# Kernel optimization log

Hardware: AMD Instinct MI355X
Metric: run time of the kernel (lower is better)

## Reference

```python
import jax, jax.numpy as jnp
import numpy as np

H8, W8 = 64, 64
H4, W4 = 128, 128
C_LAT, C_HI = 256, 128
N_Q = 1024
ORIG_H, ORIG_W = 512, 512
NUM_ITERS = 4
TEMP = 20.0
DIM = 4 + C_HI + C_LAT        # 388 mixer output dim
IN_DIM = DIM + 3 * 49         # 535 mixer input dim
HID = 512


def _unit(v):
    return v / jnp.sqrt(jnp.maximum(jnp.sum(v * v, axis=-1, keepdims=True), 1e-12))


def setup_inputs() -> dict:
    key = jax.random.key(0)
    ks = jax.random.split(key, 20)
    fg = _unit(jax.random.normal(ks[0], (1, H8, W8, C_LAT), jnp.float32))
    hg = _unit(jax.random.normal(ks[1], (1, H4, W4, C_HI), jnp.float32))
    qf = _unit(jax.random.normal(ks[2], (1, N_Q, C_LAT), jnp.float32))
    hq = _unit(jax.random.normal(ks[3], (1, N_Q, C_HI), jnp.float32))
    p = lambda k, s, sc=0.05: sc * jax.random.normal(k, s, jnp.float32)
    return dict(
        feature_grid=fg, hires_feats_grid=hg, query_feats=qf, hires_query_feats=hq,
        hid1_w=p(ks[4], (16, 1, 3, 3)), hid1_b=jnp.zeros((16,), jnp.float32),
        hid2_w=p(ks[5], (1, 16, 3, 3)), hid2_b=jnp.zeros((1,), jnp.float32),
        hid3_w=p(ks[6], (32, 16, 3, 3)), hid3_b=jnp.zeros((32,), jnp.float32),
        hid4_w=p(ks[7], (32, 16)), hid4_b=jnp.zeros((16,), jnp.float32),
        occ_w=p(ks[8], (16, 2)), occ_b=jnp.zeros((2,), jnp.float32),
        mix_in_w=p(ks[9], (IN_DIM, HID), 0.02), mix_in_b=jnp.zeros((HID,), jnp.float32),
        mix_out_w=p(ks[10], (HID, DIM), 0.02), mix_out_b=jnp.zeros((DIM,), jnp.float32),
    )


def _conv2d(x, w, b, stride, pad):
    y = jax.lax.conv_general_dilated(x, w, (stride, stride), pad,
                                     dimension_numbers=('NCHW', 'OIHW', 'NCHW'))
    return y + b[None, :, None, None]


def _bilinear_sample(grid, coords):
    # grid [H,W,C]; coords [..., 2] as (y, x); edge-clamped bilinear gather.
    H, W = grid.shape[0], grid.shape[1]
    y, x = coords[..., 0], coords[..., 1]
    y0f, x0f = jnp.floor(y), jnp.floor(x)
    wy, wx = (y - y0f)[..., None], (x - x0f)[..., None]
    y0 = jnp.clip(y0f.astype(jnp.int32), 0, H - 1)
    y1 = jnp.clip(y0f.astype(jnp.int32) + 1, 0, H - 1)
    x0 = jnp.clip(x0f.astype(jnp.int32), 0, W - 1)
    x1 = jnp.clip(x0f.astype(jnp.int32) + 1, 0, W - 1)
    g00, g01 = grid[y0, x0], grid[y0, x1]
    g10, g11 = grid[y1, x0], grid[y1, x1]
    return (g00 * (1 - wy) * (1 - wx) + g01 * (1 - wy) * wx
            + g10 * wy * (1 - wx) + g11 * wy * wx)


def _forward(fg, hg, qf, hq, hid1_w, hid1_b, hid2_w, hid2_b, hid3_w, hid3_b,
             hid4_w, hid4_b, occ_w, occ_b, mix_in_w, mix_in_b, mix_out_w, mix_out_b):
    # --- tracks_from_cost_volume ---
    cv = jnp.einsum('bnc,bhwc->bnhw', qf, fg)                 # [1,N,64,64]
    b, n, h, w = cv.shape
    x = cv.reshape(b * n, 1, h, w)
    occ_map = jax.nn.relu(_conv2d(x, hid1_w, hid1_b, 1, 'SAME'))   # [bn,16,h,w]
    pmap = _conv2d(occ_map, hid2_w, hid2_b, 1, 'SAME').reshape(b * n, h * w)
    heat = jax.nn.softmax(pmap * TEMP, axis=-1).reshape(b * n, h, w)
    ey = jnp.einsum('bhw,h->b', heat, jnp.arange(h, dtype=jnp.float32))
    ex = jnp.einsum('bhw,w->b', heat, jnp.arange(w, dtype=jnp.float32))
    points = jnp.stack([ex * (ORIG_W / w), ey * (ORIG_H / h)], -1).reshape(b, n, 2)
    op = jnp.pad(occ_map, ((0, 0), (0, 0), (0, 2), (0, 2)))
    o3 = jax.nn.relu(_conv2d(op, hid3_w, hid3_b, 2, 'VALID'))
    o3 = o3.mean((-1, -2))                                     # [bn,32]
    o3 = jax.nn.relu(o3 @ hid4_w + hid4_b)
    o3 = (o3 @ occ_w + occ_b).reshape(b, n, 2)
    occ, expd = o3[..., 0], o3[..., 1]

    # --- iterative pips refinement ---
    cy, cx = jnp.meshgrid(jnp.arange(-3, 4), jnp.arange(-3, 4), indexing='ij')
    ctx = jnp.stack([cy, cx], -1).reshape(-1, 2).astype(jnp.float32)   # [49,2] (dy,dx)
    fg_avg = fg.reshape(1, H8 // 2, 2, W8 // 2, 2, C_LAT).mean((2, 4))
    pyramid = [hg, fg, fg_avg]
    feats = jnp.concatenate([hq, qf], -1)                      # [1,N,384]
    pos = points
    for it in range(NUM_ITERS):
        if it == 0:
            queries = [hq[0], qf[0], qf[0]]
        else:
            queries = [feats[0, :, :C_HI], feats[0, :, C_HI:], feats[0, :, C_HI:]]
        corrs = []
        for grid, q in zip(pyramid, queries):
            gh, gw = grid.shape[1], grid.shape[2]
            scale = jnp.array([gw / ORIG_W, gh / ORIG_H], jnp.float32)
            c = (pos[0] * scale)[:, ::-1]                      # (x,y)->(y,x), [N,2]
            coords2 = c[:, None, :] + ctx[None]                # [N,49,2]
            nb = _bilinear_sample(grid[0], coords2)            # [N,49,C]
            corrs.append(jnp.einsum('nsc,nc->ns', nb, q))
        corrs = jnp.concatenate(corrs, -1)[None]               # [1,N,147]
        mlp_in = jnp.concatenate([jnp.zeros_like(pos), occ[..., None],
                                  expd[..., None], feats, corrs], -1)
        res = jax.nn.gelu(mlp_in @ mix_in_w + mix_in_b) @ mix_out_w + mix_out_b
        pos = pos + res[..., :2]
        occ = occ + res[..., 2]
        expd = expd + res[..., 3]
        feats = feats + res[..., 4:]
    return jnp.concatenate([pos, occ[..., None], expd[..., None]], -1)  # [1,N,4]


def reference(feature_grid, hires_feats_grid, query_feats, hires_query_feats,
              hid1_w, hid1_b, hid2_w, hid2_b, hid3_w, hid3_b, hid4_w, hid4_b,
              occ_w, occ_b, mix_in_w, mix_in_b, mix_out_w, mix_out_b):
    return _forward(feature_grid, hires_feats_grid, query_feats, hires_query_feats,
                    hid1_w, hid1_b, hid2_w, hid2_b, hid3_w, hid3_b, hid4_w, hid4_b,
                    occ_w, occ_b, mix_in_w, mix_in_b, mix_out_w, mix_out_b)
```

## Files before the change

### kernel.cpp

```cpp
#include <hip/hip_runtime.h>
#include <hip/hip_bf16.h>
#include <math.h>


#define NQ 1024
#define TEMPF 20.0f
#define DIMV 388
#define INDIM 535
#define KPAD 544
#define HID 512

#define WS_CVB     0
#define WS_WIT     2097152
#define WS_WOT     2236416
#define WS_FG16    2351104
#define WS_HG16    2875392
#define WS_AV16    3923968
#define WS_FGAVG   4194304
#define WS_POS     (WS_FGAVG + 262144)
#define WS_OCC     (WS_POS + NQ*2)
#define WS_EXPD    (WS_OCC + NQ)
#define WS_FEATS   (WS_EXPD + NQ)
#define WS_MLPIN   (WS_FEATS + NQ*384)
#define WS_HIDDEN  (WS_MLPIN + NQ*KPAD)
#define WS_W3B     (WS_HIDDEN + NQ*HID)
#define WS_W2B     (WS_W3B + 2560)
#define WS_PART    (WS_MLPIN + 278528)
#define WS_SUM3    WS_HIDDEN

#define CVP 68
#define ROWP 2368

typedef __attribute__((ext_vector_type(8))) short bf16x8;
typedef __attribute__((ext_vector_type(4))) float f32x4;

union BU8 { uint4 u; __hip_bfloat16 h[8]; };

__device__ __forceinline__ int occ_off(int r, int idx, int c) {
  int o = idx * 32 + c * 2;
  o ^= ((idx >> 2) & 3) << 4;
  return r * ROWP + o;
}

__global__ __launch_bounds__(256) void k_prep_cv(
    const float* __restrict__ fg, const float* __restrict__ hg,
    const float* __restrict__ qf, const float* __restrict__ hq,
    const float* __restrict__ w3, const float* __restrict__ w2,
    const float* __restrict__ wi, const float* __restrict__ wo,
    float* __restrict__ ws) {
  __shared__ __hip_bfloat16 A_s[32 * 32];
  __shared__ __hip_bfloat16 B_s[64 * 32];
  const int bx = blockIdx.x;
  const int t = threadIdx.x;

  if (bx >= 2048) {
    int i = (bx - 2048) * 256 + t;
    if (i < 262144) {
      int c = i & 255, ox = (i >> 8) & 31, oy = i >> 13;
      const float* b = fg + (((oy * 2) * 64 + ox * 2) << 8) + c;
      float av = 0.25f * (b[0] + b[256] + b[16384] + b[16384 + 256]);
      ((__hip_bfloat16*)(ws + WS_AV16))[i] = __float2bfloat16(av);
    } else if (i < 655360) {
      int j = i - 262144;
      int n = j / 384, c = j - n * 384;
      float v = (c < 128) ? hq[n * 128 + c] : qf[n * 256 + c - 128];
      ws[WS_FEATS + j] = v;
      __hip_bfloat16* mi = (__hip_bfloat16*)(ws + WS_MLPIN);
      mi[n * KPAD + 4 + c] = __float2bfloat16(v);
      if (c == 0) {
        mi[n * KPAD + 0] = __float2bfloat16(0.f);
        mi[n * KPAD + 1] = __float2bfloat16(0.f);
      }
    } else if (i < 660480) {
      int j = i - 655360;
      int e = j & 7, qd = (j >> 3) & 3, nl = (j >> 5) & 15;
      int nt = (j >> 9) & 1, kt = j >> 10;
      int k = kt * 32 + qd * 8 + e;
      int ic = k & 15, tap = k >> 4;
      int oc = nt * 16 + nl;
      float v = (tap < 9) ? w3[(oc * 16 + ic) * 9 + tap] : 0.f;
      ((__hip_bfloat16*)(ws + WS_W3B))[j] = __float2bfloat16(v);
    } else if (i < 663040) {
      int j = i - 660480;
      int e = j & 7, qd = (j >> 3) & 3, kt = j >> 9;
      int k = kt * 32 + qd * 8 + e;
      int ch = k & 15, tap = k >> 4;
      float v = (tap < 9) ? w2[ch * 9 + tap] : 0.f;
      ((__hip_bfloat16*)(ws + WS_W2B))[j] = __float2bfloat16(v);
    } else if (i < 1187328) {
      ws[WS_SUM3 + (i - 663040)] = 0.f;
    } else if (i < 1465856) {
      int j = i - 1187328;
      int n = j / KPAD, k = j - n * KPAD;
      float v = (k < INDIM) ? wi[k * HID + n] : 0.f;
      ((__hip_bfloat16*)(ws + WS_WIT))[j] = __float2bfloat16(v);
    } else if (i < 1695232) {
      int j = i - 1465856;
      int n = j >> 9, k = j & 511;
      float v = (n < DIMV) ? wo[k * DIMV + n] : 0.f;
      ((__hip_bfloat16*)(ws + WS_WOT))[j] = __float2bfloat16(v);
    } else if (i < 1957376) {
      int j = (i - 1695232) * 4;
      float4 v = *(const float4*)&fg[j];
      union { __hip_bfloat16 h[4]; uint2 u; } pk;
      pk.h[0] = __float2bfloat16(v.x); pk.h[1] = __float2bfloat16(v.y);
      pk.h[2] = __float2bfloat16(v.z); pk.h[3] = __float2bfloat16(v.w);
      *(uint2*)(((__hip_bfloat16*)(ws + WS_FG16)) + j) = pk.u;
    } else {
      int j = (i - 1957376) * 4;
      float4 v = *(const float4*)&hg[j];
      union { __hip_bfloat16 h[4]; uint2 u; } pk;
      pk.h[0] = __float2bfloat16(v.x); pk.h[1] = __float2bfloat16(v.y);
      pk.h[2] = __float2bfloat16(v.z); pk.h[3] = __float2bfloat16(v.w);
      *(uint2*)(((__hip_bfloat16*)(ws + WS_HG16)) + j) = pk.u;
    }
    return;
  }

  const int wv = t >> 6, lane = t & 63;
  const int wm = wv & 1, wn = wv >> 1;
  const int quad = lane >> 4, nl = lane & 15;
  const int p0 = (bx & 63) * 64, m0 = (bx >> 6) * 32;
  f32x4 acc0 = {0.f, 0.f, 0.f, 0.f};
  f32x4 acc1 = {0.f, 0.f, 0.f, 0.f};

  for (int k0 = 0; k0 < 256; k0 += 32) {
    {
      int r = t >> 3, c = t & 7;
      float4 v = *(const float4*)&qf[(m0 + r) * 256 + k0 + c * 4];
      union { __hip_bfloat16 h[4]; uint2 u; } pk;
      pk.h[0] = __float2bfloat16(v.x); pk.h[1] = __float2bfloat16(v.y);
      pk.h[2] = __float2bfloat16(v.z); pk.h[3] = __float2bfloat16(v.w);
      *(uint2*)&A_s[r * 32 + c * 4] = pk.u;
    }
    {
      int r = t >> 2, c = t & 3;
      const float* src = &fg[(p0 + r) * 256 + k0 + c * 8];
      float4 v0 = *(const float4*)src;
      float4 v1 = *(const float4*)(src + 4);
      union { __hip_bfloat16 h[8]; uint4 u; } pk;
      pk.h[0] = __float2bfloat16(v0.x); pk.h[1] = __float2bfloat16(v0.y);
      pk.h[2] = __float2bfloat16(v0.z); pk.h[3] = __float2bfloat16(v0.w);
      pk.h[4] = __float2bfloat16(v1.x); pk.h[5] = __float2bfloat16(v1.y);
      pk.h[6] = __float2bfloat16(v1.z); pk.h[7] = __float2bfloat16(v1.w);
      *(uint4*)&B_s[r * 32 + c * 8] = pk.u;
    }
    __syncthreads();
    bf16x8 a = *(const bf16x8*)&A_s[(16 * wm + nl) * 32 + quad * 8];
    bf16x8 b0 = *(const bf16x8*)&B_s[(32 * wn + nl) * 32 + quad * 8];
    bf16x8 b1 = *(const bf16x8*)&B_s[(32 * wn + 16 + nl) * 32 + quad * 8];
    acc0 = __builtin_amdgcn_mfma_f32_16x16x32_bf16(a, b0, acc0, 0, 0, 0);
    acc1 = __builtin_amdgcn_mfma_f32_16x16x32_bf16(a, b1, acc1, 0, 0, 0);
    __syncthreads();
  }
  __hip_bfloat16* cvb = (__hip_bfloat16*)ws;
#pragma unroll
  for (int nt = 0; nt < 2; nt++) {
    int n = p0 + 32 * wn + nt * 16 + nl;
#pragma unroll
    for (int r = 0; r < 4; r++) {
      int m = m0 + 16 * wm + quad * 4 + r;
      cvb[m * 4096 + n] = __float2bfloat16(nt ? acc1[r] : acc0[r]);
    }
  }
}

__global__ __launch_bounds__(256, 5) void k_head_stripe(
    const float* __restrict__ h1w, const float* __restrict__ h1b,
    const float* __restrict__ h2b, const float* __restrict__ h3b,
    float* __restrict__ ws) {
  __shared__ float cvs[8 * CVP];
  __shared__ float4 occ_t4[6 * ROWP / 16];
  char* occ_t = (char*)occ_t4;

  const int bx = blockIdx.x;
  const int q = bx >> 4, st = bx & 15;
  const int y0 = st * 4;
  const int t = threadIdx.x;
  const int wv = t >> 6, lane = t & 63;
  const int role = (wv + bx) & 3;
  const __hip_bfloat16* cvb = (const __hip_bfloat16*)ws + q * 4096;

  if (t < 192) {
    int r = t >> 5, j = t & 31;
    int off = r * ROWP + ((j < 16) ? j * 8 : 2176 + (j - 16) * 8);
    *(uint2*)(occ_t + off) = make_uint2(0u, 0u);
  }
  if (st == 0 || st == 15) {
    int r = (st == 0) ? 0 : 5;
    for (int i = t; i < 288; i += 256)
      *(uint2*)(occ_t + r * ROWP + i * 8) = make_uint2(0u, 0u);
  }
#pragma unroll
  for (int j = 0; j < 2; j++) {
    int i = t + 256 * j;
    int lr = i >> 6, x = i & 63;
    int g = y0 - 2 + lr;
    cvs[lr * CVP + x + 1] =
        (g >= 0 && g < 64) ? __bfloat162float(cvb[g * 64 + x]) : 0.f;
  }
  if (t < 32) {
    int rr = t >> 2, c = t & 3;
    cvs[rr * CVP + ((c == 0) ? 0 : (64 + c))] = 0.f;
  }
  __syncthreads();

  {
    const int x = lane;
    const int chg = wv * 4;
    float w1r[4][9], b1r[4];
#pragma unroll
    for (int k = 0; k < 4; k++) {
      b1r[k] = h1b[chg + k];
#pragma unroll
      for (int j = 0; j < 9; j++) w1r[k][j] = h1w[(chg + k) * 9 + j];
    }
    float win[3][3];
#pragma unroll
    for (int j = 0; j < 3; j++) {
      const float* cp = &cvs[j * CVP + x];
      win[j][0] = cp[0]; win[j][1] = cp[1]; win[j][2] = cp[2];
    }
    for (int r = 0; r < 6; r++) {
      if (r > 0) {
#pragma unroll
        for (int c = 0; c < 3; c++) { win[0][c] = win[1][c]; win[1][c] = win[2][c]; }
        const float* cp = &cvs[(r + 2) * CVP + x];
        win[2][0] = cp[0]; win[2][1] = cp[1]; win[2][2] = cp[2];
      }
      int yo = y0 - 1 + r;
      if (yo >= 0 && yo <= 63) {
        union { __hip_bfloat16 h[4]; uint2 u; } pk;
#pragma unroll
        for (int k = 0; k < 4; k++) {
          float a = b1r[k];
#pragma unroll
          for (int ky = 0; ky < 3; ky++)
            a += w1r[k][3 * ky] * win[ky][0] + w1r[k][3 * ky + 1] * win[ky][1] +
                 w1r[k][3 * ky + 2] * win[ky][2];
          pk.h[k] = __float2bfloat16(fmaxf(a, 0.f));
        }
        *(uint2*)(occ_t + occ_off(r, x + 4, chg)) = pk.u;
      }
    }
  }
  __syncthreads();

  const int nl = lane & 15;
  const int qd = lane >> 4, qh = qd >> 1, ql = qd & 1;

  if (role == 1 || role == 2) {
    const __hip_bfloat16* W3B = (const __hip_bfloat16*)(ws + WS_W3B);
    const int oyl = role - 1;
    f32x4 acc00 = {0.f,0.f,0.f,0.f}, acc01 = {0.f,0.f,0.f,0.f};
    f32x4 acc10 = {0.f,0.f,0.f,0.f}, acc11 = {0.f,0.f,0.f,0.f};
#pragma unroll
    for (int kt = 0; kt < 5; kt++) {
      int tap = kt * 2 + qh;
      bf16x8 a0, a1;
      if (tap < 9) {
        int ky = (tap >= 6) ? 2 : ((tap >= 3) ? 1 : 0);
        int kx = tap - 3 * ky;
        int R = 2 * oyl + 1 + ky;
        int idx0 = 4 + kx + 2 * nl;
        a0 = *(const bf16x8*)(occ_t + occ_off(R, idx0, ql * 8));
        a1 = *(const bf16x8*)(occ_t + occ_off(R, idx0 + 32, ql * 8));
      } else {
        a0 = (bf16x8){0, 0, 0, 0, 0, 0, 0, 0};
        a1 = a0;
      }
      bf16x8 b0 = *(const bf16x8*)&W3B[((kt * 2 + 0) * 16 + nl) * 32 + qd * 8];
      bf16x8 b1 = *(const bf16x8*)&W3B[((kt * 2 + 1) * 16 + nl) * 32 + qd * 8];
      acc00 = __builtin_amdgcn_mfma_f32_16x16x32_bf16(a0, b0, acc00, 0, 0, 0);
      acc01 = __builtin_amdgcn_mfma_f32_16x16x32_bf16(a0, b1, acc01, 0, 0, 0);
      acc10 = __builtin_amdgcn_mfma_f32_16x16x32_bf16(a1, b0, acc10, 0, 0, 0);
      acc11 = __builtin_amdgcn_mfma_f32_16x16x32_bf16(a1, b1, acc11, 0, 0, 0);
    }
    float bb0 = h3b[nl], bb1 = h3b[16 + nl];
    float s0 = 0.f, s1 = 0.f;
#pragma unroll
    for (int r = 0; r < 4; r++) {
      s0 += fmaxf(acc00[r] + bb0, 0.f) + fmaxf(acc10[r] + bb0, 0.f);
      s1 += fmaxf(acc01[r] + bb1, 0.f) + fmaxf(acc11[r] + bb1, 0.f);
    }
    s0 += __shfl_xor(s0, 16); s0 += __shfl_xor(s0, 32);
    s1 += __shfl_xor(s1, 16); s1 += __shfl_xor(s1, 32);
    if (lane < 16) {
      atomicAdd(&ws[WS_SUM3 + (q * 16 + st) * 32 + nl], s0);
      atomicAdd(&ws[WS_SUM3 + (q * 16 + st) * 32 + 16 + nl], s1);
    }
  } else {
    const int rl0 = (role == 3) ? 2 : 0;
    const __hip_bfloat16* W2B = (const __hip_bfloat16*)(ws + WS_W2B);
    bf16x8 wb0 = *(const bf16x8*)&W2B[(0 * 16 + nl) * 32 + qd * 8];
    bf16x8 wb1 = *(const bf16x8*)&W2B[(1 * 16 + nl) * 32 + qd * 8];
    bf16x8 wb2 = *(const bf16x8*)&W2B[(2 * 16 + nl) * 32 + qd * 8];
    bf16x8 wb3 = *(const bf16x8*)&W2B[(3 * 16 + nl) * 32 + qd * 8];
    bf16x8 wb4 = *(const bf16x8*)&W2B[(4 * 16 + nl) * 32 + qd * 8];
    f32x4 pa0 = {0.f,0.f,0.f,0.f}, pa1 = {0.f,0.f,0.f,0.f};
    f32x4 pa2 = {0.f,0.f,0.f,0.f}, pa3 = {0.f,0.f,0.f,0.f};
    f32x4 pa4 = {0.f,0.f,0.f,0.f}, pa5 = {0.f,0.f,0.f,0.f};
    f32x4 pa6 = {0.f,0.f,0.f,0.f}, pa7 = {0.f,0.f,0.f,0.f};

#define H2STEP(ACC, ROW, XT, KT, WB)                                         \
    {                                                                        \
      int tap = (KT) * 2 + qh;                                               \
      bf16x8 a;                                                              \
      if (tap < 9) {                                                         \
        int ky = (tap >= 6) ? 2 : ((tap >= 3) ? 1 : 0);                      \
        int kx = tap - 3 * ky;                                               \
        a = *(const bf16x8*)(occ_t +                                         \
            occ_off((ROW) + ky, (XT) + nl + 3 + kx, ql * 8));                \
      } else { a = (bf16x8){0, 0, 0, 0, 0, 0, 0, 0}; }                       \
      ACC = __builtin_amdgcn_mfma_f32_16x16x32_bf16(a, WB, ACC, 0, 0, 0);    \
    }
#define H2TILE(ACC, ROW, XT)                                                 \
    H2STEP(ACC, ROW, XT, 0, wb0) H2STEP(ACC, ROW, XT, 1, wb1)                \
    H2STEP(ACC, ROW, XT, 2, wb2) H2STEP(ACC, ROW, XT, 3, wb3)                \
    H2STEP(ACC, ROW, XT, 4, wb4)

    H2TILE(pa0, rl0, 0)      H2TILE(pa1, rl0, 16)
    H2TILE(pa2, rl0, 32)     H2TILE(pa3, rl0, 48)
    H2TILE(pa4, rl0 + 1, 0)  H2TILE(pa5, rl0 + 1, 16)
    H2TILE(pa6, rl0 + 1, 32) H2TILE(pa7, rl0 + 1, 48)
#undef H2TILE
#undef H2STEP

    const float bb = h2b[0];
    float mg = -1e30f;
#pragma unroll
    for (int r = 0; r < 4; r++) {
      mg = fmaxf(mg, fmaxf(fmaxf(pa0[r], pa1[r]), fmaxf(pa2[r], pa3[r])));
      mg = fmaxf(mg, fmaxf(fmaxf(pa4[r], pa5[r]), fmaxf(pa6[r], pa7[r])));
    }
    mg = (mg + bb) * TEMPF;
    mg = fmaxf(mg, __shfl_xor(mg, 16));
    mg = fmaxf(mg, __shfl_xor(mg, 32));
    float sa = 0.f, sb = 0.f, sx = 0.f;
    const float fq = (float)(qd * 4);
#pragma unroll
    for (int r = 0; r < 4; r++) {
      float xr = fq + (float)r;
      float e;
      e = __expf((pa0[r] + bb) * TEMPF - mg); sa += e; sx += e * (xr + 0.f);
      e = __expf((pa1[r] + bb) * TEMPF - mg); sa += e; sx += e * (xr + 16.f);
      e = __expf((pa2[r] + bb) * TEMPF - mg); sa += e; sx += e * (xr + 32.f);
      e = __expf((pa3[r] + bb) * TEMPF - mg); sa += e; sx += e * (xr + 48.f);
      e = __expf((pa4[r] + bb) * TEMPF - mg); sb += e; sx += e * (xr + 0.f);
      e = __expf((pa5[r] + bb) * TEMPF - mg); sb += e; sx += e * (xr + 16.f);
      e = __expf((pa6[r] + bb) * TEMPF - mg); sb += e; sx += e * (xr + 32.f);
      e = __expf((pa7[r] + bb) * TEMPF - mg); sb += e; sx += e * (xr + 48.f);
    }
    float ya = (float)(y0 + rl0);
    float s = sa + sb;
    float sy = ya * sa + (ya + 1.f) * sb;
    s += __shfl_xor(s, 16); sx += __shfl_xor(sx, 16); sy += __shfl_xor(sy, 16);
    s += __shfl_xor(s, 32); sx += __shfl_xor(sx, 32); sy += __shfl_xor(sy, 32);
    if (lane == 0) {
      int slot = q * 32 + st * 2 + ((role == 3) ? 1 : 0);
      *(float4*)&ws[WS_PART + slot * 4] = make_float4(mg, s, sx, sy);
    }
  }
}

__global__ __launch_bounds__(256) void k_merge(
    const float* __restrict__ w4, const float* __restrict__ b4,
    const float* __restrict__ w5, const float* __restrict__ b5,
    float* __restrict__ ws) {
  __shared__ float sums_s[4][32];
  __shared__ float o4s[4][16];
  int t = threadIdx.x, wv = t >> 6, lane = t & 63;
  int q = blockIdx.x * 4 + wv;

  float M = -1e30f, S = 0.f, SX = 0.f, SY = 0.f;
  if (lane < 32) {
    float4 pv = *(const float4*)&ws[WS_PART + (q * 32 + lane) * 4];
    M = pv.x; S = pv.y; SX = pv.z; SY = pv.w;
  }
#pragma unroll
  for (int off = 1; off < 64; off <<= 1) {
    float Mo = __shfl_xor(M, off), So = __shfl_xor(S, off);
    float SXo = __shfl_xor(SX, off), SYo = __shfl_xor(SY, off);
    float Mn = fmaxf(M, Mo);
    float c1 = __expf(M - Mn), c2 = __expf(Mo - Mn);
    S = S * c1 + So * c2; SX = SX * c1 + SXo * c2; SY = SY * c1 + SYo * c2;
    M = Mn;
  }
  if (lane == 0) {
    ws[WS_POS + q * 2 + 0] = (SX / S) * 8.0f;
    ws[WS_POS + q * 2 + 1] = (SY / S) * 8.0f;
  }

  int ch = lane & 31, half = lane >> 5;
  float sm = 0.f;
#pragma unroll
  for (int s8 = 0; s8 < 8; s8++)
    sm += ws[WS_SUM3 + (q * 16 + half * 8 + s8) * 32 + ch];
  sm += __shfl_xor(sm, 32);
  if (lane < 32) sums_s[wv][lane] = sm * (1.f / 1024.f);
  __syncthreads();
  if (lane < 16) {
    float a = b4[lane];
#pragma unroll
    for (int i = 0; i < 32; i++) a += sums_s[wv][i] * w4[i * 16 + lane];
    o4s[wv][lane] = fmaxf(a, 0.f);
  }
  __syncthreads();
  if (lane < 2) {
    float r = b5[lane];
#pragma unroll
    for (int j = 0; j < 16; j++) r += o4s[wv][j] * w5[j * 2 + lane];
    __hip_bfloat16* mi = (__hip_bfloat16*)(ws + WS_MLPIN);
    if (lane == 0) { ws[WS_OCC + q] = r;  mi[q * KPAD + 2] = __float2bfloat16(r); }
    else           { ws[WS_EXPD + q] = r; mi[q * KPAD + 3] = __float2bfloat16(r); }
  }
}

__global__ __launch_bounds__(256) void k_corr(float* __restrict__ ws) {
  __shared__ float qs[384];
  __shared__ float dbuf[3][64];
  int t = threadIdx.x;
  int wv = t >> 6, lane = t & 63;
  int cl = lane & 15, sub = lane >> 4;
  int n = blockIdx.x;
  const float* feats = ws + WS_FEATS + n * 384;
  float posx = ws[WS_POS + n * 2 + 0];
  float posy = ws[WS_POS + n * 2 + 1];
  __hip_bfloat16* mi = (__hip_bfloat16*)(ws + WS_MLPIN) + n * KPAD;

  for (int col = t; col < 384; col += 256) qs[col] = feats[col];
  __syncthreads();

  float qh[8], qq[16];
#pragma unroll
  for (int j = 0; j < 8; j++) qh[j] = qs[cl * 8 + j];
#pragma unroll
  for (int j = 0; j < 16; j++) qq[j] = qs[128 + cl * 16 + j];

  const __hip_bfloat16* G0 = (const __hip_bfloat16*)(ws + WS_HG16);
  const __hip_bfloat16* G1 = (const __hip_bfloat16*)(ws + WS_FG16);
  const __hip_bfloat16* G2 = (const __hip_bfloat16*)(ws + WS_AV16);

#pragma unroll
  for (int L = 0; L < 3; L++) {
    const __hip_bfloat16* grid;
    int Hg, Wg;
    float scl;
    if (L == 0)      { grid = G0; Hg = 128; Wg = 128; scl = 0.25f; }
    else if (L == 1) { grid = G1; Hg = 64;  Wg = 64;  scl = 0.125f; }
    else             { grid = G2; Hg = 32;  Wg = 32;  scl = 0.0625f; }
    float cy = posy * scl, cx = posx * scl;
    int iy = (int)floorf(cy), ix = (int)floorf(cx);
#pragma unroll
    for (int g = 0; g < 4; g++) {
      int p = wv * 16 + g * 4 + sub;
      int a = p >> 3, b = p & 7;
      int row = iy + a - 3; row = row < 0 ? 0 : (row > Hg - 1 ? Hg - 1 : row);
      int col = ix + b - 3; col = col < 0 ? 0 : (col > Wg - 1 ? Wg - 1 : col);
      float acc = 0.f;
      if (L == 0) {
        BU8 g0; g0.u = *(const uint4*)(grid + (row * Wg + col) * 128 + cl * 8);
#pragma unroll
        for (int j = 0; j < 8; j++) acc += __bfloat162float(g0.h[j]) * qh[j];
      } else {
        const __hip_bfloat16* gp = grid + (row * Wg + col) * 256 + cl * 16;
        BU8 g0, g1;
        g0.u = *(const uint4*)gp;
        g1.u = *(const uint4*)(gp + 8);
#pragma unroll
        for (int j = 0; j < 8; j++) {
          acc += __bfloat162float(g0.h[j]) * qq[j];
          acc += __bfloat162float(g1.h[j]) * qq[8 + j];
        }
      }
      acc += __shfl_xor(acc, 1);
      acc += __shfl_xor(acc, 2);
      acc += __shfl_xor(acc, 4);
      acc += __shfl_xor(acc, 8);
      if (cl == 0) dbuf[L][p] = acc;
    }
  }
  __syncthreads();

  if (t < 147) {
    int L = t / 49, s = t - L * 49;
    int sa = s / 7, sb = s - sa * 7;
    float scl = (L == 0) ? 0.25f : ((L == 1) ? 0.125f : 0.0625f);
    float cy = posy * scl, cx = posx * scl;
    float wy = cy - floorf(cy), wx = cx - floorf(cx);
    int i00 = sa * 8 + sb;
    float d00 = dbuf[L][i00], d01 = dbuf[L][i00 + 1];
    float d10 = dbuf[L][i00 + 8], d11 = dbuf[L][i00 + 9];
    float corr = (1.f - wy) * (1.f - wx) * d00 + (1.f - wy) * wx * d01 +
                 wy * (1.f - wx) * d10 + wy * wx * d11;
    mi[388 + t] = __float2bfloat16(corr);
  }
}

__device__ __forceinline__ float gelu_tanh(float x) {
  float z = 0.7978845608028654f * (x + 0.044715f * x * x * x);
  z = fminf(fmaxf(z, -15.f), 15.f);
  float e = __expf(2.f * z);
  float th = (e - 1.f) / (e + 1.f);
  return 0.5f * x * (1.f + th);
}

__global__ __launch_bounds__(256) void k_mix1(
    const float* __restrict__ bias, float* __restrict__ ws) {
  const int t = threadIdx.x;
  const int wv = t >> 6, lane = t & 63;
  const int nt = blockIdx.x * 4 + wv;
  const int mt = blockIdx.y;
  const int m0 = mt * 16, n0 = nt * 16;
  const int nl = lane & 15, quad = lane >> 4;
  const unsigned short* Abf = (const unsigned short*)(ws + WS_MLPIN);
  const unsigned short* WIT = (const unsigned short*)(ws + WS_WIT);
  const unsigned short* ap = &Abf[(m0 + nl) * KPAD + quad * 8];
  const unsigned short* bp = &WIT[(n0 + nl) * KPAD + quad * 8];
  f32x4 acc = {0.f, 0.f, 0.f, 0.f};
#pragma unroll
  for (int ks = 0; ks < 17; ks++) {
    bf16x8 a = *(const bf16x8*)(ap + ks * 32);
    bf16x8 b = *(const bf16x8*)(bp + ks * 32);
    acc = __builtin_amdgcn_mfma_f32_16x16x32_bf16(a, b, acc, 0, 0, 0);
  }
  __hip_bfloat16* Hd = (__hip_bfloat16*)(ws + WS_HIDDEN);
  int nn = n0 + nl;
  float bv = bias[nn];
#pragma unroll
  for (int r = 0; r < 4; r++) {
    int m = m0 + quad * 4 + r;
    Hd[m * HID + nn] = __float2bfloat16(gelu_tanh(acc[r] + bv));
  }
}

__global__ __launch_bounds__(256) void k_mix2(
    const float* __restrict__ bias, float* __restrict__ ws,
    float* __restrict__ out) {
  const int t = threadIdx.x;
  const int wv = t >> 6, lane = t & 63;
  const int nt = blockIdx.x * 4 + wv;
  const int mt = blockIdx.y;
  const int m0 = mt * 16, n0 = nt * 16;
  const int nl = lane & 15, quad = lane >> 4;
  const unsigned short* Abf = (const unsigned short*)(ws + WS_HIDDEN);
  const unsigned short* WOT = (const unsigned short*)(ws + WS_WOT);
  const unsigned short* ap = &Abf[(m0 + nl) * HID + quad * 8];
  const unsigned short* bp = &WOT[(n0 + nl) * HID + quad * 8];
  f32x4 acc = {0.f, 0.f, 0.f, 0.f};
#pragma unroll
  for (int ks = 0; ks < 16; ks++) {
    bf16x8 a = *(const bf16x8*)(ap + ks * 32);
    bf16x8 b = *(const bf16x8*)(bp + ks * 32);
    acc = __builtin_amdgcn_mfma_f32_16x16x32_bf16(a, b, acc, 0, 0, 0);
  }

  int col = n0 + nl;
  if (col < DIMV) {
    float bv = bias[col];
    __hip_bfloat16* mib = (__hip_bfloat16*)(ws + WS_MLPIN);
#pragma unroll
    for (int r = 0; r < 4; r++) {
      int m = m0 + quad * 4 + r;
      float rr = acc[r] + bv;
      if (col < 2) {
        float v = ws[WS_POS + m * 2 + col] + rr;
        ws[WS_POS + m * 2 + col] = v;
        out[m * 4 + col] = v;
      } else if (col == 2) {
        float v = ws[WS_OCC + m] + rr;
        ws[WS_OCC + m] = v;
        out[m * 4 + 2] = v;
        mib[m * KPAD + 2] = __float2bfloat16(v);
      } else if (col == 3) {
        float v = ws[WS_EXPD + m] + rr;
        ws[WS_EXPD + m] = v;
        out[m * 4 + 3] = v;
        mib[m * KPAD + 3] = __float2bfloat16(v);
      } else {
        float v = ws[WS_FEATS + m * 384 + (col - 4)] + rr;
        ws[WS_FEATS + m * 384 + (col - 4)] = v;
        mib[m * KPAD + col] = __float2bfloat16(v);
      }
    }
  }
}

extern "C" void kernel_launch(void* const* d_in, const int* in_sizes, int n_in,
                              void* d_out, int out_size, void* d_ws, size_t ws_size,
                              hipStream_t stream) {
  const float* fg = (const float*)d_in[0];
  const float* hg = (const float*)d_in[1];
  const float* qf = (const float*)d_in[2];
  const float* hq = (const float*)d_in[3];
  const float* w1 = (const float*)d_in[4];
  const float* b1 = (const float*)d_in[5];
  const float* w2 = (const float*)d_in[6];
  const float* b2 = (const float*)d_in[7];
  const float* w3 = (const float*)d_in[8];
  const float* b3 = (const float*)d_in[9];
  const float* w4 = (const float*)d_in[10];
  const float* b4 = (const float*)d_in[11];
  const float* w5 = (const float*)d_in[12];
  const float* b5 = (const float*)d_in[13];
  const float* wi = (const float*)d_in[14];
  const float* bi = (const float*)d_in[15];
  const float* wo = (const float*)d_in[16];
  const float* bo = (const float*)d_in[17];
  float* ws = (float*)d_ws;
  float* out = (float*)d_out;

  k_prep_cv<<<11742, 256, 0, stream>>>(fg, hg, qf, hq, w3, w2, wi, wo, ws);
  k_head_stripe<<<16384, 256, 0, stream>>>(w1, b1, b2, b3, ws);
  k_merge<<<256, 256, 0, stream>>>(w4, b4, w5, b5, ws);
  for (int it = 0; it < 4; it++) {
    k_corr<<<1024, 256, 0, stream>>>(ws);
    k_mix1<<<dim3(8, 64), 256, 0, stream>>>(bi, ws);
    k_mix2<<<dim3(7, 64), 256, 0, stream>>>(bo, ws, out);
  }
}
```

Measured before the change: 298.2 us.

## Fuse merge, correlation and mixer MLP iterations into one persistent kernel

Replaces the merge kernel and the four-iteration loop of correlation, mixer-in and mixer-out launches with a single kernel where each block owns 8 queries and keeps their state, MLP inputs and hidden activations in LDS. This removes many kernel launches and the global round trips for intermediate buffers between stages. In exchange only 128 blocks run, half of each 16-row MFMA tile is padding, and every block re-streams the full mixer weight matrices from L2 each iteration.

```diff
diff --git a/kernel.cpp b/kernel.cpp
--- a/kernel.cpp
+++ b/kernel.cpp
@@ -30,6 +30,8 @@
 
 #define CVP 68
 #define ROWP 2368
+#define MIP 552
+#define HP  520
 
 typedef __attribute__((ext_vector_type(8))) short bf16x8;
 typedef __attribute__((ext_vector_type(4))) float f32x4;
@@ -363,140 +365,6 @@
   }
 }
 
-__global__ __launch_bounds__(256) void k_merge(
-    const float* __restrict__ w4, const float* __restrict__ b4,
-    const float* __restrict__ w5, const float* __restrict__ b5,
-    float* __restrict__ ws) {
-  __shared__ float sums_s[4][32];
-  __shared__ float o4s[4][16];
-  int t = threadIdx.x, wv = t >> 6, lane = t & 63;
-  int q = blockIdx.x * 4 + wv;
-
-  float M = -1e30f, S = 0.f, SX = 0.f, SY = 0.f;
-  if (lane < 32) {
-    float4 pv = *(const float4*)&ws[WS_PART + (q * 32 + lane) * 4];
-    M = pv.x; S = pv.y; SX = pv.z; SY = pv.w;
-  }
-#pragma unroll
-  for (int off = 1; off < 64; off <<= 1) {
-    float Mo = __shfl_xor(M, off), So = __shfl_xor(S, off);
-    float SXo = __shfl_xor(SX, off), SYo = __shfl_xor(SY, off);
-    float Mn = fmaxf(M, Mo);
-    float c1 = __expf(M - Mn), c2 = __expf(Mo - Mn);
-    S = S * c1 + So * c2; SX = SX * c1 + SXo * c2; SY = SY * c1 + SYo * c2;
-    M = Mn;
-  }
-  if (lane == 0) {
-    ws[WS_POS + q * 2 + 0] = (SX / S) * 8.0f;
-    ws[WS_POS + q * 2 + 1] = (SY / S) * 8.0f;
-  }
-
-  int ch = lane & 31, half = lane >> 5;
-  float sm = 0.f;
-#pragma unroll
-  for (int s8 = 0; s8 < 8; s8++)
-    sm += ws[WS_SUM3 + (q * 16 + half * 8 + s8) * 32 + ch];
-  sm += __shfl_xor(sm, 32);
-  if (lane < 32) sums_s[wv][lane] = sm * (1.f / 1024.f);
-  __syncthreads();
-  if (lane < 16) {
-    float a = b4[lane];
-#pragma unroll
-    for (int i = 0; i < 32; i++) a += sums_s[wv][i] * w4[i * 16 + lane];
-    o4s[wv][lane] = fmaxf(a, 0.f);
-  }
-  __syncthreads();
-  if (lane < 2) {
-    float r = b5[lane];
-#pragma unroll
-    for (int j = 0; j < 16; j++) r += o4s[wv][j] * w5[j * 2 + lane];
-    __hip_bfloat16* mi = (__hip_bfloat16*)(ws + WS_MLPIN);
-    if (lane == 0) { ws[WS_OCC + q] = r;  mi[q * KPAD + 2] = __float2bfloat16(r); }
-    else           { ws[WS_EXPD + q] = r; mi[q * KPAD + 3] = __float2bfloat16(r); }
-  }
-}
-
-__global__ __launch_bounds__(256) void k_corr(float* __restrict__ ws) {
-  __shared__ float qs[384];
-  __shared__ float dbuf[3][64];
-  int t = threadIdx.x;
-  int wv = t >> 6, lane = t & 63;
-  int cl = lane & 15, sub = lane >> 4;
-  int n = blockIdx.x;
-  const float* feats = ws + WS_FEATS + n * 384;
-  float posx = ws[WS_POS + n * 2 + 0];
-  float posy = ws[WS_POS + n * 2 + 1];
-  __hip_bfloat16* mi = (__hip_bfloat16*)(ws + WS_MLPIN) + n * KPAD;
-
-  for (int col = t; col < 384; col += 256) qs[col] = feats[col];
-  __syncthreads();
-
-  float qh[8], qq[16];
-#pragma unroll
-  for (int j = 0; j < 8; j++) qh[j] = qs[cl * 8 + j];
-#pragma unroll
-  for (int j = 0; j < 16; j++) qq[j] = qs[128 + cl * 16 + j];
-
-  const __hip_bfloat16* G0 = (const __hip_bfloat16*)(ws + WS_HG16);
-  const __hip_bfloat16* G1 = (const __hip_bfloat16*)(ws + WS_FG16);
-  const __hip_bfloat16* G2 = (const __hip_bfloat16*)(ws + WS_AV16);
-
-#pragma unroll
-  for (int L = 0; L < 3; L++) {
-    const __hip_bfloat16* grid;
-    int Hg, Wg;
-    float scl;
-    if (L == 0)      { grid = G0; Hg = 128; Wg = 128; scl = 0.25f; }
-    else if (L == 1) { grid = G1; Hg = 64;  Wg = 64;  scl = 0.125f; }
-    else             { grid = G2; Hg = 32;  Wg = 32;  scl = 0.0625f; }
-    float cy = posy * scl, cx = posx * scl;
-    int iy = (int)floorf(cy), ix = (int)floorf(cx);
-#pragma unroll
-    for (int g = 0; g < 4; g++) {
-      int p = wv * 16 + g * 4 + sub;
-      int a = p >> 3, b = p & 7;
-      int row = iy + a - 3; row = row < 0 ? 0 : (row > Hg - 1 ? Hg - 1 : row);
-      int col = ix + b - 3; col = col < 0 ? 0 : (col > Wg - 1 ? Wg - 1 : col);
-      float acc = 0.f;
-      if (L == 0) {
-        BU8 g0; g0.u = *(const uint4*)(grid + (row * Wg + col) * 128 + cl * 8);
-#pragma unroll
-        for (int j = 0; j < 8; j++) acc += __bfloat162float(g0.h[j]) * qh[j];
-      } else {
-        const __hip_bfloat16* gp = grid + (row * Wg + col) * 256 + cl * 16;
-        BU8 g0, g1;
-        g0.u = *(const uint4*)gp;
-        g1.u = *(const uint4*)(gp + 8);
-#pragma unroll
-        for (int j = 0; j < 8; j++) {
-          acc += __bfloat162float(g0.h[j]) * qq[j];
-          acc += __bfloat162float(g1.h[j]) * qq[8 + j];
-        }
-      }
-      acc += __shfl_xor(acc, 1);
-      acc += __shfl_xor(acc, 2);
-      acc += __shfl_xor(acc, 4);
-      acc += __shfl_xor(acc, 8);
-      if (cl == 0) dbuf[L][p] = acc;
-    }
-  }
-  __syncthreads();
-
-  if (t < 147) {
-    int L = t / 49, s = t - L * 49;
-    int sa = s / 7, sb = s - sa * 7;
-    float scl = (L == 0) ? 0.25f : ((L == 1) ? 0.125f : 0.0625f);
-    float cy = posy * scl, cx = posx * scl;
-    float wy = cy - floorf(cy), wx = cx - floorf(cx);
-    int i00 = sa * 8 + sb;
-    float d00 = dbuf[L][i00], d01 = dbuf[L][i00 + 1];
-    float d10 = dbuf[L][i00 + 8], d11 = dbuf[L][i00 + 9];
-    float corr = (1.f - wy) * (1.f - wx) * d00 + (1.f - wy) * wx * d01 +
-                 wy * (1.f - wx) * d10 + wy * wx * d11;
-    mi[388 + t] = __float2bfloat16(corr);
-  }
-}
-
 __device__ __forceinline__ float gelu_tanh(float x) {
   float z = 0.7978845608028654f * (x + 0.044715f * x * x * x);
   z = fminf(fmaxf(z, -15.f), 15.f);
@@ -505,84 +373,259 @@
   return 0.5f * x * (1.f + th);
 }
 
-__global__ __launch_bounds__(256) void k_mix1(
-    const float* __restrict__ bias, float* __restrict__ ws) {
+__global__ __launch_bounds__(256) void k_refine(
+    const float* __restrict__ w4, const float* __restrict__ b4,
+    const float* __restrict__ w5, const float* __restrict__ b5,
+    const float* __restrict__ bi, const float* __restrict__ bo,
+    float* __restrict__ ws, float* __restrict__ out) {
+  __shared__ __align__(16) __hip_bfloat16 mi_s[16 * MIP];
+  __shared__ __align__(16) char hv[16 * HP * 2];
+  __shared__ __align__(16) float feats_s[8][384];
+  __shared__ float pos_s[8][2];
+  __shared__ float occ_s[8], expd_s[8];
+  __shared__ float sums_r[4][32];
+  __shared__ float o4_r[4][16];
+  __hip_bfloat16* hidden_s = (__hip_bfloat16*)hv;
+  float* dbuf = (float*)hv;
+
   const int t = threadIdx.x;
   const int wv = t >> 6, lane = t & 63;
-  const int nt = blockIdx.x * 4 + wv;
-  const int mt = blockIdx.y;
-  const int m0 = mt * 16, n0 = nt * 16;
+  const int q0 = blockIdx.x * 8;
   const int nl = lane & 15, quad = lane >> 4;
-  const unsigned short* Abf = (const unsigned short*)(ws + WS_MLPIN);
+
+  {
+    const __hip_bfloat16* mig = (const __hip_bfloat16*)(ws + WS_MLPIN);
+    for (int j = t; j < 544; j += 256) {
+      int r = j / 68, c = j - r * 68;
+      *(uint4*)&mi_s[r * MIP + c * 8] =
+          *(const uint4*)&mig[(q0 + r) * KPAD + c * 8];
+    }
+    uint* z = (uint*)&mi_s[8 * MIP];
+    for (int j = t; j < 2208; j += 256) z[j] = 0u;
+    for (int j = t; j < 768; j += 256) {
+      int r = j / 96, c = j - r * 96;
+      *(float4*)&feats_s[r][c * 4] =
+          *(const float4*)&ws[WS_FEATS + (q0 + r) * 384 + c * 4];
+    }
+  }
+  for (int rep = 0; rep < 2; ++rep) {
+    int qi = wv * 2 + rep;
+    int q = q0 + qi;
+    float M = -1e30f, S = 0.f, SX = 0.f, SY = 0.f;
+    if (lane < 32) {
+      float4 pv = *(const float4*)&ws[WS_PART + (q * 32 + lane) * 4];
+      M = pv.x; S = pv.y; SX = pv.z; SY = pv.w;
+    }
+#pragma unroll
+    for (int off = 1; off < 64; off <<= 1) {
+      float Mo = __shfl_xor(M, off), So = __shfl_xor(S, off);
+      float SXo = __shfl_xor(SX, off), SYo = __shfl_xor(SY, off);
+      float Mn = fmaxf(M, Mo);
+      float c1 = __expf(M - Mn), c2 = __expf(Mo - Mn);
+      S = S * c1 + So * c2; SX = SX * c1 + SXo * c2; SY = SY * c1 + SYo * c2;
+      M = Mn;
+    }
+    if (lane == 0) {
+      pos_s[qi][0] = (SX / S) * 8.0f;
+      pos_s[qi][1] = (SY / S) * 8.0f;
+    }
+    int ch = lane & 31, half = lane >> 5;
+    float sm = 0.f;
+#pragma unroll
+    for (int s8 = 0; s8 < 8; s8++)
+      sm += ws[WS_SUM3 + (q * 16 + half * 8 + s8) * 32 + ch];
+    sm += __shfl_xor(sm, 32);
+    if (lane < 32) sums_r[wv][lane] = sm * (1.f / 1024.f);
+    __syncthreads();
+    if (lane < 16) {
+      float a = b4[lane];
+#pragma unroll
+      for (int i = 0; i < 32; i++) a += sums_r[wv][i] * w4[i * 16 + lane];
+      o4_r[wv][lane] = fmaxf(a, 0.f);
+    }
+    __syncthreads();
+    if (lane < 2) {
+      float r = b5[lane];
+#pragma unroll
+      for (int j = 0; j < 16; j++) r += o4_r[wv][j] * w5[j * 2 + lane];
+      if (lane == 0) { occ_s[qi] = r;  mi_s[qi * MIP + 2] = __float2bfloat16(r); }
+      else           { expd_s[qi] = r; mi_s[qi * MIP + 3] = __float2bfloat16(r); }
+    }
+    __syncthreads();
+  }
+
+  const __hip_bfloat16* G0 = (const __hip_bfloat16*)(ws + WS_HG16);
+  const __hip_bfloat16* G1 = (const __hip_bfloat16*)(ws + WS_FG16);
+  const __hip_bfloat16* G2 = (const __hip_bfloat16*)(ws + WS_AV16);
   const unsigned short* WIT = (const unsigned short*)(ws + WS_WIT);
-  const unsigned short* ap = &Abf[(m0 + nl) * KPAD + quad * 8];
-  const unsigned short* bp = &WIT[(n0 + nl) * KPAD + quad * 8];
-  f32x4 acc = {0.f, 0.f, 0.f, 0.f};
-#pragma unroll
-  for (int ks = 0; ks < 17; ks++) {
-    bf16x8 a = *(const bf16x8*)(ap + ks * 32);
-    bf16x8 b = *(const bf16x8*)(bp + ks * 32);
-    acc = __builtin_amdgcn_mfma_f32_16x16x32_bf16(a, b, acc, 0, 0, 0);
-  }
-  __hip_bfloat16* Hd = (__hip_bfloat16*)(ws + WS_HIDDEN);
-  int nn = n0 + nl;
-  float bv = bias[nn];
-#pragma unroll
-  for (int r = 0; r < 4; r++) {
-    int m = m0 + quad * 4 + r;
-    Hd[m * HID + nn] = __float2bfloat16(gelu_tanh(acc[r] + bv));
-  }
-}
-
-__global__ __launch_bounds__(256) void k_mix2(
-    const float* __restrict__ bias, float* __restrict__ ws,
-    float* __restrict__ out) {
-  const int t = threadIdx.x;
-  const int wv = t >> 6, lane = t & 63;
-  const int nt = blockIdx.x * 4 + wv;
-  const int mt = blockIdx.y;
-  const int m0 = mt * 16, n0 = nt * 16;
-  const int nl = lane & 15, quad = lane >> 4;
-  const unsigned short* Abf = (const unsigned short*)(ws + WS_HIDDEN);
   const unsigned short* WOT = (const unsigned short*)(ws + WS_WOT);
-  const unsigned short* ap = &Abf[(m0 + nl) * HID + quad * 8];
-  const unsigned short* bp = &WOT[(n0 + nl) * HID + quad * 8];
-  f32x4 acc = {0.f, 0.f, 0.f, 0.f};
-#pragma unroll
-  for (int ks = 0; ks < 16; ks++) {
-    bf16x8 a = *(const bf16x8*)(ap + ks * 32);
-    bf16x8 b = *(const bf16x8*)(bp + ks * 32);
-    acc = __builtin_amdgcn_mfma_f32_16x16x32_bf16(a, b, acc, 0, 0, 0);
-  }
-
-  int col = n0 + nl;
-  if (col < DIMV) {
-    float bv = bias[col];
-    __hip_bfloat16* mib = (__hip_bfloat16*)(ws + WS_MLPIN);
-#pragma unroll
-    for (int r = 0; r < 4; r++) {
-      int m = m0 + quad * 4 + r;
-      float rr = acc[r] + bv;
-      if (col < 2) {
-        float v = ws[WS_POS + m * 2 + col] + rr;
-        ws[WS_POS + m * 2 + col] = v;
-        out[m * 4 + col] = v;
-      } else if (col == 2) {
-        float v = ws[WS_OCC + m] + rr;
-        ws[WS_OCC + m] = v;
-        out[m * 4 + 2] = v;
-        mib[m * KPAD + 2] = __float2bfloat16(v);
-      } else if (col == 3) {
-        float v = ws[WS_EXPD + m] + rr;
-        ws[WS_EXPD + m] = v;
-        out[m * 4 + 3] = v;
-        mib[m * KPAD + 3] = __float2bfloat16(v);
-      } else {
-        float v = ws[WS_FEATS + m * 384 + (col - 4)] + rr;
-        ws[WS_FEATS + m * 384 + (col - 4)] = v;
-        mib[m * KPAD + col] = __float2bfloat16(v);
-      }
-    }
+  const int cq = t >> 5, sl = t & 31;
+  const int cl = sl & 15, ph = sl >> 4;
+
+  for (int it = 0; it < 4; ++it) {
+    {
+      float posx = pos_s[cq][0], posy = pos_s[cq][1];
+      float qh[8], qq[16];
+#pragma unroll
+      for (int j = 0; j < 8; j++) qh[j] = feats_s[cq][cl * 8 + j];
+#pragma unroll
+      for (int j = 0; j < 16; j++) qq[j] = feats_s[cq][128 + cl * 16 + j];
+      float* db = dbuf + cq * 192;
+#pragma unroll
+      for (int L = 0; L < 3; L++) {
+        const __hip_bfloat16* grid;
+        int Hg, Wg;
+        float scl;
+        if (L == 0)      { grid = G0; Hg = 128; Wg = 128; scl = 0.25f; }
+        else if (L == 1) { grid = G1; Hg = 64;  Wg = 64;  scl = 0.125f; }
+        else             { grid = G2; Hg = 32;  Wg = 32;  scl = 0.0625f; }
+        float cy = posy * scl, cx = posx * scl;
+        int iy = (int)floorf(cy), ix = (int)floorf(cx);
+        for (int p2 = 0; p2 < 32; ++p2) {
+          int p = p2 * 2 + ph;
+          int a = p >> 3, b = p & 7;
+          int row = iy + a - 3; row = row < 0 ? 0 : (row > Hg - 1 ? Hg - 1 : row);
+          int col = ix + b - 3; col = col < 0 ? 0 : (col > Wg - 1 ? Wg - 1 : col);
+          float acc = 0.f;
+          if (L == 0) {
+            BU8 g0; g0.u = *(const uint4*)(grid + (row * Wg + col) * 128 + cl * 8);
+#pragma unroll
+            for (int j = 0; j < 8; j++) acc += __bfloat162float(g0.h[j]) * qh[j];
+          } else {
+            const __hip_bfloat16* gp = grid + (row * Wg + col) * 256 + cl * 16;
+            BU8 g0, g1;
+            g0.u = *(const uint4*)gp;
+            g1.u = *(const uint4*)(gp + 8);
+#pragma unroll
+            for (int j = 0; j < 8; j++) {
+              acc += __bfloat162float(g0.h[j]) * qq[j];
+              acc += __bfloat162float(g1.h[j]) * qq[8 + j];
+            }
+          }
+          acc += __shfl_xor(acc, 1);
+          acc += __shfl_xor(acc, 2);
+          acc += __shfl_xor(acc, 4);
+          acc += __shfl_xor(acc, 8);
+          if (cl == 0) db[L * 64 + p] = acc;
+        }
+      }
+    }
+    __syncthreads();
+    for (int j = t; j < 8 * 147; j += 256) {
+      int qi = j / 147, s = j - qi * 147;
+      int L = s / 49, ss = s - L * 49;
+      int sa = ss / 7, sb = ss - sa * 7;
+      float scl = (L == 0) ? 0.25f : ((L == 1) ? 0.125f : 0.0625f);
+      float cy = pos_s[qi][1] * scl, cx = pos_s[qi][0] * scl;
+      float wy = cy - floorf(cy), wx = cx - floorf(cx);
+      const float* db = dbuf + qi * 192 + L * 64;
+      int i00 = sa * 8 + sb;
+      float d00 = db[i00], d01 = db[i00 + 1];
+      float d10 = db[i00 + 8], d11 = db[i00 + 9];
+      float corr = (1.f - wy) * (1.f - wx) * d00 + (1.f - wy) * wx * d01 +
+                   wy * (1.f - wx) * d10 + wy * wx * d11;
+      mi_s[qi * MIP + 388 + s] = __float2bfloat16(corr);
+    }
+    __syncthreads();
+    {
+      bf16x8 af[17];
+#pragma unroll
+      for (int j = 0; j < 17; j++)
+        af[j] = *(const bf16x8*)&mi_s[nl * MIP + j * 32 + quad * 8];
+#pragma unroll
+      for (int tp = 0; tp < 4; ++tp) {
+        int n0a = (wv * 8 + tp * 2) * 16;
+        int n0b = n0a + 16;
+        const unsigned short* bpa = &WIT[(n0a + nl) * KPAD + quad * 8];
+        const unsigned short* bpb = &WIT[(n0b + nl) * KPAD + quad * 8];
+        f32x4 aca = {0.f, 0.f, 0.f, 0.f}, acb = {0.f, 0.f, 0.f, 0.f};
+#pragma unroll
+        for (int ks = 0; ks < 17; ks++) {
+          bf16x8 ba = *(const bf16x8*)(bpa + ks * 32);
+          bf16x8 bb = *(const bf16x8*)(bpb + ks * 32);
+          aca = __builtin_amdgcn_mfma_f32_16x16x32_bf16(af[ks], ba, aca, 0, 0, 0);
+          acb = __builtin_amdgcn_mfma_f32_16x16x32_bf16(af[ks], bb, acb, 0, 0, 0);
+        }
+        float bva = bi[n0a + nl], bvb = bi[n0b + nl];
+#pragma unroll
+        for (int r = 0; r < 4; r++) {
+          hidden_s[(quad * 4 + r) * HP + n0a + nl] =
+              __float2bfloat16(gelu_tanh(aca[r] + bva));
+          hidden_s[(quad * 4 + r) * HP + n0b + nl] =
+              __float2bfloat16(gelu_tanh(acb[r] + bvb));
+        }
+      }
+    }
+    __syncthreads();
+    {
+      bf16x8 ag[16];
+#pragma unroll
+      for (int j = 0; j < 16; j++)
+        ag[j] = *(const bf16x8*)&hidden_s[nl * HP + j * 32 + quad * 8];
+
+#define M2EPI(ACC, N0)                                                        \
+      {                                                                       \
+        int col = (N0) + nl;                                                  \
+        if (col < DIMV) {                                                     \
+          float bv = bo[col];                                                 \
+          _Pragma("unroll")                                                   \
+          for (int r = 0; r < 4; r++) {                                       \
+            int qi = quad * 4 + r;                                            \
+            if (qi < 8) {                                                     \
+              float rr = ACC[r] + bv;                                         \
+              if (col < 2) {                                                  \
+                float v = pos_s[qi][col] + rr;                                \
+                pos_s[qi][col] = v;                                           \
+                if (it == 3) out[(q0 + qi) * 4 + col] = v;                    \
+              } else if (col == 2) {                                          \
+                float v = occ_s[qi] + rr; occ_s[qi] = v;                      \
+                if (it == 3) out[(q0 + qi) * 4 + 2] = v;                      \
+                mi_s[qi * MIP + 2] = __float2bfloat16(v);                     \
+              } else if (col == 3) {                                          \
+                float v = expd_s[qi] + rr; expd_s[qi] = v;                    \
+                if (it == 3) out[(q0 + qi) * 4 + 3] = v;                      \
+                mi_s[qi * MIP + 3] = __float2bfloat16(v);                     \
+              } else {                                                        \
+                float v = feats_s[qi][col - 4] + rr;                          \
+                feats_s[qi][col - 4] = v;                                     \
+                mi_s[qi * MIP + col] = __float2bfloat16(v);                   \
+              }                                                               \
+            }                                                                 \
+          }                                                                   \
+        }                                                                     \
+      }
+
+#pragma unroll
+      for (int tp = 0; tp < 3; ++tp) {
+        int n0a = (wv * 7 + tp * 2) * 16;
+        int n0b = n0a + 16;
+        const unsigned short* bpa = &WOT[(n0a + nl) * HID + quad * 8];
+        const unsigned short* bpb = &WOT[(n0b + nl) * HID + quad * 8];
+        f32x4 aca = {0.f, 0.f, 0.f, 0.f}, acb = {0.f, 0.f, 0.f, 0.f};
+#pragma unroll
+        for (int ks = 0; ks < 16; ks++) {
+          bf16x8 ba = *(const bf16x8*)(bpa + ks * 32);
+          bf16x8 bb = *(const bf16x8*)(bpb + ks * 32);
+          aca = __builtin_amdgcn_mfma_f32_16x16x32_bf16(ag[ks], ba, aca, 0, 0, 0);
+          acb = __builtin_amdgcn_mfma_f32_16x16x32_bf16(ag[ks], bb, acb, 0, 0, 0);
+        }
+        M2EPI(aca, n0a)
+        M2EPI(acb, n0b)
+      }
+      {
+        int n0 = (wv * 7 + 6) * 16;
+        const unsigned short* bp = &WOT[(n0 + nl) * HID + quad * 8];
+        f32x4 acc = {0.f, 0.f, 0.f, 0.f};
+#pragma unroll
+        for (int ks = 0; ks < 16; ks++) {
+          bf16x8 b = *(const bf16x8*)(bp + ks * 32);
+          acc = __builtin_amdgcn_mfma_f32_16x16x32_bf16(ag[ks], b, acc, 0, 0, 0);
+        }
+        M2EPI(acc, n0)
+      }
+#undef M2EPI
+    }
+    __syncthreads();
   }
 }
 
@@ -612,10 +655,5 @@
 
   k_prep_cv<<<11742, 256, 0, stream>>>(fg, hg, qf, hq, w3, w2, wi, wo, ws);
   k_head_stripe<<<16384, 256, 0, stream>>>(w1, b1, b2, b3, ws);
-  k_merge<<<256, 256, 0, stream>>>(w4, b4, w5, b5, ws);
-  for (int it = 0; it < 4; it++) {
-    k_corr<<<1024, 256, 0, stream>>>(ws);
-    k_mix1<<<dim3(8, 64), 256, 0, stream>>>(bi, ws);
-    k_mix2<<<dim3(7, 64), 256, 0, stream>>>(bo, ws, out);
-  }
+  k_refine<<<128, 256, 0, stream>>>(w4, b4, w5, b5, bi, bo, ws, out);
 }
```

New measurement: 648.4 us. +117.4%, slower.
